# Performance work log

Measured on AMD Instinct MI355X. Metric: run time of the kernel, lower is better.

The kernel has to match this reference:

```python
import jax, jax.numpy as jnp
import numpy as np

B, IN_DIM, UNITS = 16384, 3072, 3072  # batch, input_dim=3*unit1, units=3*unit2


def setup_inputs() -> dict:
    key = jax.random.key(0)
    k1, k2, k3 = jax.random.split(key, 3)
    inputs = jax.random.normal(k1, (B, IN_DIM), dtype=jnp.float32)
    # original init: uniform [0, 0.01) for w, zeros for b (gpe_bias = [0, 0])
    w = jax.random.uniform(k2, (IN_DIM, UNITS), dtype=jnp.float32, minval=0.0, maxval=0.01)
    b = jnp.zeros((UNITS,), dtype=jnp.float32)
    # per-unit binary diagonal mask, stored as [units, input_dim]
    mask = jax.random.randint(k3, (UNITS, IN_DIM), 0, 2, dtype=jnp.int32)
    return {"inputs": inputs, "w": w, "b": b, "mask": mask}


def reference(inputs, w, b, mask):
    # Original: p = transpose(s @ inputs^T, [2,0,1]) -> [batch, units, input_dim]
    #           f = diag_part(p @ w) + b            -> [batch, units]
    # Since s[u] = diag(mask[u]), this is exactly:
    #   f[b,u] = sum_i inputs[b,i] * mask[u,i] * w[i,u] + b[u]
    # i.e. a single masked GEMM with effective weight w * mask^T.
    w_eff = w * mask.T.astype(w.dtype)  # [input_dim, units]
    return inputs @ w_eff + b
```

## Files before the change

### kernel.cpp

```cpp
#include <hip/hip_runtime.h>

#define BATCH 16384
#define KDIM  3072
#define NDIM  3072

typedef __bf16 bf16;
typedef bf16  bf16x8  __attribute__((ext_vector_type(8)));
typedef float f32x16  __attribute__((ext_vector_type(16)));

__device__ __forceinline__ void g2l16(const bf16* g, bf16* l) {
    __builtin_amdgcn_global_load_lds(
        (__attribute__((address_space(1))) unsigned int*)g,
        (__attribute__((address_space(3))) unsigned int*)l,
        16, 0, 0);
}

__global__ __launch_bounds__(256) void cvt_a_kernel(const float* __restrict__ in,
                                                    bf16* __restrict__ out) {
    const long idx = (long)blockIdx.x * 256 + threadIdx.x;
    const float4* in4 = (const float4*)in;
    float4 a = in4[idx * 2];
    float4 b = in4[idx * 2 + 1];
    bf16x8 o;
    o[0] = (bf16)a.x; o[1] = (bf16)a.y; o[2] = (bf16)a.z; o[3] = (bf16)a.w;
    o[4] = (bf16)b.x; o[5] = (bf16)b.y; o[6] = (bf16)b.z; o[7] = (bf16)b.w;
    ((bf16x8*)out)[idx] = o;
}

__global__ __launch_bounds__(256) void weff_kernel(const float* __restrict__ w,
                                                   const int* __restrict__ mask,
                                                   bf16* __restrict__ wt) {
    __shared__ float tile[32][33];
    const int i0 = blockIdx.x * 32;
    const int u0 = blockIdx.y * 32;
    const int tx = threadIdx.x, ty = threadIdx.y;
#pragma unroll
    for (int r = 0; r < 4; r++)
        tile[ty + 8 * r][tx] = w[(long)(i0 + ty + 8 * r) * NDIM + u0 + tx];
    __syncthreads();
#pragma unroll
    for (int r = 0; r < 4; r++) {
        int u = u0 + ty + 8 * r;
        int i = i0 + tx;
        float v = tile[tx][ty + 8 * r] * (float)mask[(long)u * KDIM + i];
        wt[(long)u * KDIM + i] = (bf16)v;
    }
}

__global__ __launch_bounds__(512, 2) void gemm_kernel(const bf16* __restrict__ A,
                                                      const bf16* __restrict__ Bt,
                                                      const float* __restrict__ bias,
                                                      float* __restrict__ C) {
    __shared__ __align__(16) bf16 lds[2 * 32768];

    const int tid  = threadIdx.x;
    const int lane = tid & 63;
    const int wv   = tid >> 6;
    const int rl   = lane & 31;
    const int kb   = lane >> 5;
    const int sx   = rl & 7;

    const int lid = blockIdx.y * gridDim.x + blockIdx.x;
    const int sid = (lid & 7) * 96 + (lid >> 3);
    const long m0 = (long)(sid / 12) * 256;
    const long n0 = (long)(sid % 12) * 256;

    const int waveM = (wv >> 2) * 128;
    const int waveN = (wv & 3) * 64;

    const int srow = tid >> 3;
    const int sc   = (tid & 7) ^ (srow & 7);
    const bf16* gA = A  + (m0 + srow) * KDIM + sc * 8;
    const bf16* gB = Bt + (n0 + srow) * KDIM + sc * 8;
    bf16* const dA = &lds[tid * 8];
    bf16* const dB = &lds[16384 + tid * 8];

    const int aBase = (waveM + rl) * 64;
    const int bBase = 16384 + (waveN + rl) * 64;

    f32x16 acc[4][2] = {};

    auto STAGE = [&](int p, int kt) {
        const long ko = (long)kt * 64;
        bf16* da = dA + p * 32768;
        bf16* db = dB + p * 32768;
#pragma unroll
        for (int j = 0; j < 4; ++j) g2l16(gA + (long)(64 * j) * KDIM + ko, da + j * 4096);
#pragma unroll
        for (int j = 0; j < 4; ++j) g2l16(gB + (long)(64 * j) * KDIM + ko, db + j * 4096);
    };

    auto COMPUTE = [&](const bf16* bp) {
        bf16x8 af[2][4], bfr[2][2];
        {
            const int c = kb ^ sx;
#pragma unroll
            for (int mi = 0; mi < 4; ++mi)
                af[0][mi] = *(const bf16x8*)(bp + aBase + mi * 2048 + c * 8);
#pragma unroll
            for (int ni = 0; ni < 2; ++ni)
                bfr[0][ni] = *(const bf16x8*)(bp + bBase + ni * 2048 + c * 8);
        }
#pragma unroll
        for (int ks = 0; ks < 4; ++ks) {
            const int cur = ks & 1, nxt = cur ^ 1;
            if (ks < 3) {
                const int c = ((ks + 1) * 2 + kb) ^ sx;
#pragma unroll
                for (int mi = 0; mi < 4; ++mi)
                    af[nxt][mi] = *(const bf16x8*)(bp + aBase + mi * 2048 + c * 8);
#pragma unroll
                for (int ni = 0; ni < 2; ++ni)
                    bfr[nxt][ni] = *(const bf16x8*)(bp + bBase + ni * 2048 + c * 8);
            }
            __builtin_amdgcn_s_setprio(1);
#pragma unroll
            for (int mi = 0; mi < 4; ++mi)
#pragma unroll
                for (int ni = 0; ni < 2; ++ni)
                    acc[mi][ni] = __builtin_amdgcn_mfma_f32_32x32x16_bf16(
                        af[cur][mi], bfr[cur][ni], acc[mi][ni], 0, 0, 0);
            __builtin_amdgcn_s_setprio(0);
        }
    };

    const int NT = KDIM / 64;
    STAGE(0, 0);
    STAGE(1, 1);

#pragma unroll 2
    for (int i = 0; i < NT - 2; ++i) {
        const int p = i & 1;
        asm volatile("s_waitcnt vmcnt(8)" ::: "memory");
        __builtin_amdgcn_s_barrier();
        asm volatile("" ::: "memory");
        COMPUTE(&lds[p * 32768]);
        asm volatile("s_waitcnt lgkmcnt(0)" ::: "memory");
        __builtin_amdgcn_s_barrier();
        asm volatile("" ::: "memory");
        STAGE(p, i + 2);
    }
    asm volatile("s_waitcnt vmcnt(8)" ::: "memory");
    __builtin_amdgcn_s_barrier();
    asm volatile("" ::: "memory");
    COMPUTE(&lds[0]);
    asm volatile("s_waitcnt vmcnt(0)" ::: "memory");
    __builtin_amdgcn_s_barrier();
    asm volatile("" ::: "memory");
    COMPUTE(&lds[32768]);

#pragma unroll
    for (int ni = 0; ni < 2; ++ni) {
        const long col = n0 + waveN + ni * 32 + rl;
        const float bv = bias[col];
#pragma unroll
        for (int mi = 0; mi < 4; ++mi) {
            const long rbase = m0 + waveM + mi * 32 + 4 * kb;
#pragma unroll
            for (int g = 0; g < 4; ++g)
#pragma unroll
                for (int t = 0; t < 4; ++t)
                    C[(rbase + 8 * g + t) * NDIM + col] = acc[mi][ni][4 * g + t] + bv;
        }
    }
}

__global__ __launch_bounds__(256) void naive_kernel(const float* __restrict__ x,
                                                    const float* __restrict__ w,
                                                    const float* __restrict__ bias,
                                                    const int* __restrict__ mask,
                                                    float* __restrict__ out) {
    const long idx = (long)blockIdx.x * 256 + threadIdx.x;
    const long bi = idx / NDIM;
    const int u = (int)(idx % NDIM);
    float s = 0.f;
    for (int k = 0; k < KDIM; k++)
        s += x[bi * KDIM + k] * w[(long)k * NDIM + u] * (float)mask[(long)u * KDIM + k];
    out[idx] = s + bias[u];
}

extern "C" void kernel_launch(void* const* d_in, const int* in_sizes, int n_in,
                              void* d_out, int out_size, void* d_ws, size_t ws_size,
                              hipStream_t stream) {
    const float* x    = (const float*)d_in[0];
    const float* w    = (const float*)d_in[1];
    const float* bias = (const float*)d_in[2];
    const int*   mask = (const int*)d_in[3];
    float* out = (float*)d_out;

    const size_t needA = (size_t)BATCH * KDIM * sizeof(bf16);
    const size_t needW = (size_t)NDIM * KDIM * sizeof(bf16);

    if (ws_size < needA + needW) {
        const long total = (long)BATCH * NDIM;
        naive_kernel<<<(int)(total / 256), 256, 0, stream>>>(x, w, bias, mask, out);
        return;
    }

    bf16* Abf = (bf16*)d_ws;
    bf16* Wt  = (bf16*)((char*)d_ws + needA);

    cvt_a_kernel<<<(BATCH * (KDIM / 8)) / 256, 256, 0, stream>>>(x, Abf);
    weff_kernel<<<dim3(KDIM / 32, NDIM / 32), dim3(32, 8), 0, stream>>>(w, mask, Wt);
    gemm_kernel<<<dim3(NDIM / 256, BATCH / 256), 512, 0, stream>>>(Abf, Wt, bias, out);
}
```

Baseline: 690.0 us.

## Interleave per-k-substep global-to-LDS staging with MFMA phases in GEMM mainloop

Result: no change. 684.4 us (-0.8%).

```diff
diff --git a/kernel.cpp b/kernel.cpp
--- a/kernel.cpp
+++ b/kernel.cpp
@@ -47,6 +47,46 @@
     }
 }
 
+
+#define STAGE_UNIT(Q, KT, KS) do {                                              \
+    const long ko_ = (long)(KT) * 64 + ((KS) >> 1) * 32;                        \
+    const bf16* gs_ = (((KS) & 1) == 0) ? gA : gB;                              \
+    bf16* ds_ = &lds[(Q) * 32768 + ((((KS) & 1) == 0) ? 0 : 16384)              \
+                     + ((KS) >> 1) * 8192 + tid * 8];                           \
+    g2l16(gs_ + ko_, ds_);                                                      \
+    g2l16(gs_ + ko_ + (long)128 * KDIM, ds_ + 4096);                            \
+} while (0)
+
+#define PHASE(KS, P, DOSTAGE, KT, VM) do {                                      \
+    asm volatile("" ::: "memory");       \
+    const bf16* bp_ = &lds[(P) * 32768];                                        \
+    const int cOff_ = ((KS) >> 1) * 8192 + (((((KS) & 1) * 2) + kb) ^ sx3) * 8; \
+    bf16x8 a0_ = *(const bf16x8*)(bp_ + aOff0 + cOff_);                         \
+    bf16x8 a1_ = *(const bf16x8*)(bp_ + aOff1 + cOff_);                         \
+    bf16x8 a2_ = *(const bf16x8*)(bp_ + aOff2 + cOff_);                         \
+    bf16x8 a3_ = *(const bf16x8*)(bp_ + aOff3 + cOff_);                         \
+    bf16x8 b0_ = *(const bf16x8*)(bp_ + bOff0 + cOff_);                         \
+    bf16x8 b1_ = *(const bf16x8*)(bp_ + bOff1 + cOff_);                         \
+    if (DOSTAGE) { STAGE_UNIT((P) ^ 1, KT, KS); }                               \
+    asm volatile("" ::: "memory");          \
+    __builtin_amdgcn_s_barrier();                                               \
+    asm volatile("s_waitcnt lgkmcnt(0)" ::: "memory");                          \
+    __builtin_amdgcn_sched_barrier(0);   \
+    __builtin_amdgcn_s_setprio(1);                                              \
+    acc[0][0] = __builtin_amdgcn_mfma_f32_32x32x16_bf16(a0_, b0_, acc[0][0], 0, 0, 0); \
+    acc[0][1] = __builtin_amdgcn_mfma_f32_32x32x16_bf16(a0_, b1_, acc[0][1], 0, 0, 0); \
+    acc[1][0] = __builtin_amdgcn_mfma_f32_32x32x16_bf16(a1_, b0_, acc[1][0], 0, 0, 0); \
+    acc[1][1] = __builtin_amdgcn_mfma_f32_32x32x16_bf16(a1_, b1_, acc[1][1], 0, 0, 0); \
+    acc[2][0] = __builtin_amdgcn_mfma_f32_32x32x16_bf16(a2_, b0_, acc[2][0], 0, 0, 0); \
+    acc[2][1] = __builtin_amdgcn_mfma_f32_32x32x16_bf16(a2_, b1_, acc[2][1], 0, 0, 0); \
+    acc[3][0] = __builtin_amdgcn_mfma_f32_32x32x16_bf16(a3_, b0_, acc[3][0], 0, 0, 0); \
+    acc[3][1] = __builtin_amdgcn_mfma_f32_32x32x16_bf16(a3_, b1_, acc[3][1], 0, 0, 0); \
+    __builtin_amdgcn_s_setprio(0);                                              \
+    if ((VM) >= 0)                                                              \
+        asm volatile("s_waitcnt vmcnt(%0)" :: "n"((VM) < 0 ? 0 : (VM)) : "memory"); \
+    __builtin_amdgcn_s_barrier();                                               \
+} while (0)
+
 __global__ __launch_bounds__(512, 2) void gemm_kernel(const bf16* __restrict__ A,
                                                       const bf16* __restrict__ Bt,
                                                       const float* __restrict__ bias,
@@ -58,7 +98,7 @@
     const int wv   = tid >> 6;
     const int rl   = lane & 31;
     const int kb   = lane >> 5;
-    const int sx   = rl & 7;
+    const int sx3  = rl & 3;
 
     const int lid = blockIdx.y * gridDim.x + blockIdx.x;
     const int sid = (lid & 7) * 96 + (lid >> 3);
@@ -68,86 +108,40 @@
     const int waveM = (wv >> 2) * 128;
     const int waveN = (wv & 3) * 64;
 
-    const int srow = tid >> 3;
-    const int sc   = (tid & 7) ^ (srow & 7);
+    const int srow = tid >> 2;
+    const int sc   = (tid & 3) ^ (srow & 3);
     const bf16* gA = A  + (m0 + srow) * KDIM + sc * 8;
     const bf16* gB = Bt + (n0 + srow) * KDIM + sc * 8;
-    bf16* const dA = &lds[tid * 8];
-    bf16* const dB = &lds[16384 + tid * 8];
-
-    const int aBase = (waveM + rl) * 64;
-    const int bBase = 16384 + (waveN + rl) * 64;
+
+    const int aOff0 = (waveM + 0 * 32 + rl) * 32;
+    const int aOff1 = (waveM + 1 * 32 + rl) * 32;
+    const int aOff2 = (waveM + 2 * 32 + rl) * 32;
+    const int aOff3 = (waveM + 3 * 32 + rl) * 32;
+    const int bOff0 = 16384 + (waveN + 0 * 32 + rl) * 32;
+    const int bOff1 = 16384 + (waveN + 1 * 32 + rl) * 32;
 
     f32x16 acc[4][2] = {};
 
-    auto STAGE = [&](int p, int kt) {
-        const long ko = (long)kt * 64;
-        bf16* da = dA + p * 32768;
-        bf16* db = dB + p * 32768;
-#pragma unroll
-        for (int j = 0; j < 4; ++j) g2l16(gA + (long)(64 * j) * KDIM + ko, da + j * 4096);
-#pragma unroll
-        for (int j = 0; j < 4; ++j) g2l16(gB + (long)(64 * j) * KDIM + ko, db + j * 4096);
-    };
-
-    auto COMPUTE = [&](const bf16* bp) {
-        bf16x8 af[2][4], bfr[2][2];
-        {
-            const int c = kb ^ sx;
-#pragma unroll
-            for (int mi = 0; mi < 4; ++mi)
-                af[0][mi] = *(const bf16x8*)(bp + aBase + mi * 2048 + c * 8);
-#pragma unroll
-            for (int ni = 0; ni < 2; ++ni)
-                bfr[0][ni] = *(const bf16x8*)(bp + bBase + ni * 2048 + c * 8);
-        }
-#pragma unroll
-        for (int ks = 0; ks < 4; ++ks) {
-            const int cur = ks & 1, nxt = cur ^ 1;
-            if (ks < 3) {
-                const int c = ((ks + 1) * 2 + kb) ^ sx;
-#pragma unroll
-                for (int mi = 0; mi < 4; ++mi)
-                    af[nxt][mi] = *(const bf16x8*)(bp + aBase + mi * 2048 + c * 8);
-#pragma unroll
-                for (int ni = 0; ni < 2; ++ni)
-                    bfr[nxt][ni] = *(const bf16x8*)(bp + bBase + ni * 2048 + c * 8);
-            }
-            __builtin_amdgcn_s_setprio(1);
-#pragma unroll
-            for (int mi = 0; mi < 4; ++mi)
-#pragma unroll
-                for (int ni = 0; ni < 2; ++ni)
-                    acc[mi][ni] = __builtin_amdgcn_mfma_f32_32x32x16_bf16(
-                        af[cur][mi], bfr[cur][ni], acc[mi][ni], 0, 0, 0);
-            __builtin_amdgcn_s_setprio(0);
-        }
-    };
+    STAGE_UNIT(0, 0, 0);
+    STAGE_UNIT(0, 0, 1);
+    STAGE_UNIT(0, 0, 2);
+    STAGE_UNIT(0, 0, 3);
+    asm volatile("s_waitcnt vmcnt(4)" ::: "memory");
+    __builtin_amdgcn_s_barrier();
 
     const int NT = KDIM / 64;
-    STAGE(0, 0);
-    STAGE(1, 1);
-
 #pragma unroll 2
-    for (int i = 0; i < NT - 2; ++i) {
-        const int p = i & 1;
-        asm volatile("s_waitcnt vmcnt(8)" ::: "memory");
-        __builtin_amdgcn_s_barrier();
-        asm volatile("" ::: "memory");
-        COMPUTE(&lds[p * 32768]);
-        asm volatile("s_waitcnt lgkmcnt(0)" ::: "memory");
-        __builtin_amdgcn_s_barrier();
-        asm volatile("" ::: "memory");
-        STAGE(p, i + 2);
-    }
-    asm volatile("s_waitcnt vmcnt(8)" ::: "memory");
-    __builtin_amdgcn_s_barrier();
-    asm volatile("" ::: "memory");
-    COMPUTE(&lds[0]);
-    asm volatile("s_waitcnt vmcnt(0)" ::: "memory");
-    __builtin_amdgcn_s_barrier();
-    asm volatile("" ::: "memory");
-    COMPUTE(&lds[32768]);
+    for (int t = 0; t < NT - 1; ++t) {
+        const int p = t & 1;
+        PHASE(0, p, 1, t + 1, -1);
+        PHASE(1, p, 1, t + 1, 4);
+        PHASE(2, p, 1, t + 1, -1);
+        PHASE(3, p, 1, t + 1, 4);
+    }
+    PHASE(0, 1, 0, 0, -1);
+    PHASE(1, 1, 0, 0, 0);
+    PHASE(2, 1, 0, 0, -1);
+    PHASE(3, 1, 0, 0, -1);
 
 #pragma unroll
     for (int ni = 0; ni < 2; ++ni) {
```
